# Kernel optimization log

Hardware: AMD Instinct MI355X
Metric: run time of the kernel (lower is better)

The kernel has to match this reference:

```python
import jax, jax.numpy as jnp
import numpy as np

B, S, IN = 1, 50000, 128
N = B * S
E = 800000
HID, HEADS, OUT = 64, 2, 64
NEG_SLOPE = 0.2
BN_EPS = 1e-5


def setup_inputs() -> dict:
    key = jax.random.key(0)
    ks = jax.random.split(key, 12)
    s = 0.1
    return {
        "data": jax.random.normal(ks[0], (B, S, IN), jnp.float32),
        "edge_index": jax.random.randint(ks[1], (2, E), 0, N, dtype=jnp.int64),
        "W0": jax.random.normal(ks[2], (IN, HEADS * HID), jnp.float32) * s,
        "att_src0": jax.random.normal(ks[3], (HEADS, HID), jnp.float32) * s,
        "att_dst0": jax.random.normal(ks[4], (HEADS, HID), jnp.float32) * s,
        "bias0": jnp.zeros((HEADS * HID,), jnp.float32),
        "gamma0": jnp.ones((HEADS * HID,), jnp.float32),
        "beta0": jnp.zeros((HEADS * HID,), jnp.float32),
        "W1": jax.random.normal(ks[5], (HEADS * HID, OUT), jnp.float32) * s,
        "att_src1": jax.random.normal(ks[6], (1, OUT), jnp.float32) * s,
        "att_dst1": jax.random.normal(ks[7], (1, OUT), jnp.float32) * s,
        "bias1": jnp.zeros((OUT,), jnp.float32),
    }


def gat_conv(x, edge_index, W, att_src, att_dst, bias, heads, ch, concat):
    n = x.shape[0]
    loop = jnp.arange(n, dtype=edge_index.dtype)
    src = jnp.concatenate([edge_index[0], loop])  # PyG adds self-loops by default
    dst = jnp.concatenate([edge_index[1], loop])
    h = (x @ W).reshape(n, heads, ch)  # [N,H,C]
    a_src = (h * att_src).sum(-1)  # [N,H]
    a_dst = (h * att_dst).sum(-1)  # [N,H]
    e = jax.nn.leaky_relu(a_src[src] + a_dst[dst], NEG_SLOPE)  # [Etot,H]
    m = jax.ops.segment_max(e, dst, num_segments=n)  # segment softmax over dst
    ex = jnp.exp(e - m[dst])
    denom = jax.ops.segment_sum(ex, dst, num_segments=n)
    alpha = ex / (denom[dst] + 1e-16)  # [Etot,H]
    out = jax.ops.segment_sum(h[src] * alpha[:, :, None], dst, num_segments=n)  # [N,H,C]
    out = out.reshape(n, heads * ch) if concat else out.mean(axis=1)
    return out + bias


def reference(data, edge_index, W0, att_src0, att_dst0, bias0, gamma0, beta0,
              W1, att_src1, att_dst1, bias1):
    x = data.reshape(N, IN)
    x = gat_conv(x, edge_index, W0, att_src0, att_dst0, bias0, HEADS, HID, True)
    mu = x.mean(axis=0)
    var = x.var(axis=0)
    x = (x - mu) * jax.lax.rsqrt(var + BN_EPS) * gamma0 + beta0  # BatchNorm1d (batch stats)
    x = jax.nn.elu(x)
    x = gat_conv(x, edge_index, W1, att_src1, att_dst1, bias1, 1, OUT, False)
    return x.reshape(B, S, OUT)
```

## Files before the change

kernel.cpp:

```cpp
#include <hip/hip_runtime.h>
#include <hip/hip_fp16.h>
#include <math.h>

#define N_NODES 50000
#define E_EDGES 800000
#define NEG_SLOPE 0.2f
#define BN_EPS 1e-5f

#define BK_SHIFT 9
#define NBK 98
#define L1_BLOCKS 256
#define L1_CHUNK (E_EDGES / L1_BLOCKS)
#define CNT_N (NBK * L1_BLOCKS)
#define SCG_BLOCKS ((CNT_N + 1023) / 1024)
#define STAGE_MAX 9216

typedef __attribute__((ext_vector_type(8))) _Float16 half8;
typedef __attribute__((ext_vector_type(4))) float f32x4;

__device__ __forceinline__ float lrelu(float v) { return v > 0.f ? v : NEG_SLOPE * v; }

__global__ void k_zero(float* __restrict__ bn_sum, float* __restrict__ bn_sumsq) {
  int t = threadIdx.x;
  if (t < 128) { bn_sum[t] = 0.f; bn_sumsq[t] = 0.f; }
}

__global__ void k_cvtW(const float* __restrict__ W0, const float* __restrict__ W1,
                       _Float16* __restrict__ W0t, _Float16* __restrict__ W1t) {
  int t = threadIdx.x;
  for (int idx = t; idx < 128 * 128; idx += 256) {
    int k = idx >> 7, c = idx & 127;
    W0t[c * 128 + k] = (_Float16)W0[idx];
  }
  for (int idx = t; idx < 128 * 64; idx += 256) {
    int k = idx >> 6, c = idx & 63;
    W1t[c * 128 + k] = (_Float16)W1[idx];
  }
}

__global__ __launch_bounds__(256) void k_l1hist(const int* __restrict__ dst,
                                                int* __restrict__ cnt) {
  __shared__ int lcnt[NBK];
  int t = threadIdx.x;
  if (t < NBK) lcnt[t] = 0;
  __syncthreads();
  int beg = blockIdx.x * L1_CHUNK, end = beg + L1_CHUNK;
  for (int e = beg + t; e < end; e += 256)
    atomicAdd(&lcnt[((unsigned int)dst[e]) >> BK_SHIFT], 1);
  __syncthreads();
  for (int b = t; b < NBK; b += 256) cnt[b * L1_BLOCKS + blockIdx.x] = lcnt[b];
}

__global__ __launch_bounds__(256) void k_scan1g(const int* __restrict__ cnt,
                                                int* __restrict__ tmp,
                                                int* __restrict__ bsums) {
  __shared__ int ts[256];
  int t = threadIdx.x;
  int base = blockIdx.x * 1024 + t * 4;
  int c0 = (base + 0 < CNT_N) ? cnt[base + 0] : 0;
  int c1 = (base + 1 < CNT_N) ? cnt[base + 1] : 0;
  int c2 = (base + 2 < CNT_N) ? cnt[base + 2] : 0;
  int c3 = (base + 3 < CNT_N) ? cnt[base + 3] : 0;
  int s = c0 + c1 + c2 + c3;
  ts[t] = s;
  __syncthreads();
  for (int off = 1; off < 256; off <<= 1) {
    int v = (t >= off) ? ts[t - off] : 0;
    __syncthreads();
    ts[t] += v;
    __syncthreads();
  }
  int excl = ts[t] - s;
  if (t == 255) bsums[blockIdx.x] = ts[255];
  if (base + 0 < CNT_N) tmp[base + 0] = excl;
  if (base + 1 < CNT_N) tmp[base + 1] = excl + c0;
  if (base + 2 < CNT_N) tmp[base + 2] = excl + c0 + c1;
  if (base + 3 < CNT_N) tmp[base + 3] = excl + c0 + c1 + c2;
}

__global__ void k_scan2g(int* __restrict__ bsums) {
  int t = threadIdx.x;
  int orig = (t < SCG_BLOCKS) ? bsums[t] : 0;
  int v = orig;
#pragma unroll
  for (int off = 1; off < 64; off <<= 1) {
    int u = __shfl_up(v, off);
    if (t >= off) v += u;
  }
  if (t < SCG_BLOCKS) bsums[t] = v - orig;
}

__global__ __launch_bounds__(256) void k_l1scatter(const int* __restrict__ src,
                                                   const int* __restrict__ dst,
                                                   const int* __restrict__ tmp,
                                                   const int* __restrict__ bsums,
                                                   unsigned int* __restrict__ binned) {
  __shared__ int cur[NBK];
  int t = threadIdx.x;
  for (int b = t; b < NBK; b += 256) {
    int idx = b * L1_BLOCKS + blockIdx.x;
    cur[b] = tmp[idx] + bsums[idx >> 10];
  }
  __syncthreads();
  int beg = blockIdx.x * L1_CHUNK, end = beg + L1_CHUNK;
  for (int e = beg + t; e < end; e += 256) {
    unsigned int d = (unsigned int)dst[e];
    int b = d >> BK_SHIFT;
    int p = atomicAdd(&cur[b], 1);
    binned[p] = ((unsigned int)src[e] << 16) | d;
  }
}

__global__ void k_bbase(const int* __restrict__ tmp, const int* __restrict__ bsums,
                        int* __restrict__ bucket_base) {
  int b = threadIdx.x;
  if (b < NBK) {
    int idx = b * L1_BLOCKS;
    bucket_base[b] = tmp[idx] + bsums[idx >> 10];
  }
  if (b == NBK) bucket_base[NBK] = E_EDGES;
}

__global__ __launch_bounds__(256) void k_scatter3(const int* __restrict__ bucket_base,
                                                  const unsigned int* __restrict__ binned,
                                                  int* __restrict__ row_ptr,
                                                  int* __restrict__ csr_src) {
  __shared__ int cnt[512];
  __shared__ int staging[STAGE_MAX];
  __shared__ int ts[256];
  int t = threadIdx.x;
  int b = blockIdx.x;
  int lo = b << BK_SHIFT;
  int hi = lo + 512; if (hi > N_NODES) hi = N_NODES;
  int nloc = hi - lo;
  int base = bucket_base[b];
  int end = bucket_base[b + 1];
  cnt[t] = 0; cnt[t + 256] = 0;
  __syncthreads();
  for (int i = base + t; i < end; i += 256)
    atomicAdd(&cnt[(binned[i] & 0xFFFFu) - lo], 1);
  __syncthreads();
  int c0 = cnt[2 * t], c1 = cnt[2 * t + 1];
  int pair = c0 + c1;
  ts[t] = pair;
  __syncthreads();
  for (int off = 1; off < 256; off <<= 1) {
    int v = (t >= off) ? ts[t - off] : 0;
    __syncthreads();
    ts[t] += v;
    __syncthreads();
  }
  int exclp = ts[t] - pair;
  cnt[2 * t] = exclp;
  cnt[2 * t + 1] = exclp + c0;
  if (2 * t < nloc) row_ptr[lo + 2 * t] = base + exclp;
  if (2 * t + 1 < nloc) row_ptr[lo + 2 * t + 1] = base + exclp + c0;
  if (b == NBK - 1 && t == 0) row_ptr[N_NODES] = E_EDGES;
  __syncthreads();
  for (int i = base + t; i < end; i += 256) {
    unsigned int v = binned[i];
    int d = (int)(v & 0xFFFFu) - lo;
    int p = atomicAdd(&cnt[d], 1);
    int s = (int)(v >> 16);
    if (p < STAGE_MAX) staging[p] = s;
    else csr_src[base + p] = s;
  }
  __syncthreads();
  int tot = end - base;
  int lim = tot < STAGE_MAX ? tot : STAGE_MAX;
  for (int k = t; k < lim; k += 256) csr_src[base + k] = staging[k];
}

__global__ __launch_bounds__(256) void k_gemm0m(
    const float* __restrict__ x, const _Float16* __restrict__ Wt,
    const float* __restrict__ att_s, const float* __restrict__ att_d,
    _Float16* __restrict__ h, float* __restrict__ a_src, float* __restrict__ a_dst) {
  int lane = threadIdx.x & 63;
  int wv = threadIdx.x >> 6;
  int row0 = blockIdx.x * 64 + wv * 16;
  int m = lane & 15, kg = lane >> 4;
  int arow = row0 + m;
  int arowc = arow < N_NODES ? arow : N_NODES - 1;
  f32x4 acc[8];
#pragma unroll
  for (int ct = 0; ct < 8; ct++) acc[ct] = (f32x4){0.f, 0.f, 0.f, 0.f};
#pragma unroll
  for (int kc = 0; kc < 4; kc++) {
    const float* xp = &x[(size_t)arowc * 128 + kc * 32 + kg * 8];
    float4 xa = *(const float4*)xp;
    float4 xb = *(const float4*)(xp + 4);
    half8 af = {(_Float16)xa.x, (_Float16)xa.y, (_Float16)xa.z, (_Float16)xa.w,
                (_Float16)xb.x, (_Float16)xb.y, (_Float16)xb.z, (_Float16)xb.w};
#pragma unroll
    for (int ct = 0; ct < 8; ct++) {
      half8 bf = *(const half8*)&Wt[(ct * 16 + m) * 128 + kc * 32 + kg * 8];
      acc[ct] = __builtin_amdgcn_mfma_f32_16x16x32_f16(af, bf, acc[ct], 0, 0, 0);
    }
  }
  float as[8], ad[8];
#pragma unroll
  for (int ct = 0; ct < 8; ct++) { as[ct] = att_s[ct * 16 + m]; ad[ct] = att_d[ct * 16 + m]; }
#pragma unroll
  for (int r = 0; r < 4; r++) {
    int row = row0 + kg * 4 + r;
    bool ok = row < N_NODES;
    float ps0 = 0.f, pd0 = 0.f, ps1 = 0.f, pd1 = 0.f;
#pragma unroll
    for (int ct = 0; ct < 4; ct++) { ps0 += acc[ct][r] * as[ct]; pd0 += acc[ct][r] * ad[ct]; }
#pragma unroll
    for (int ct = 4; ct < 8; ct++) { ps1 += acc[ct][r] * as[ct]; pd1 += acc[ct][r] * ad[ct]; }
#pragma unroll
    for (int msk = 1; msk <= 8; msk <<= 1) {
      ps0 += __shfl_xor(ps0, msk); pd0 += __shfl_xor(pd0, msk);
      ps1 += __shfl_xor(ps1, msk); pd1 += __shfl_xor(pd1, msk);
    }
    if (ok) {
#pragma unroll
      for (int ct = 0; ct < 8; ct++)
        h[(size_t)row * 128 + ct * 16 + m] = (_Float16)acc[ct][r];
      if (m == 0) {
        a_src[row * 2 + 0] = ps0; a_dst[row * 2 + 0] = pd0;
        a_src[row * 2 + 1] = ps1; a_dst[row * 2 + 1] = pd1;
      }
    }
  }
}

__global__ __launch_bounds__(256) void k_gemm1m(
    const float* __restrict__ y, const float* __restrict__ scale,
    const float* __restrict__ shift, const _Float16* __restrict__ Wt,
    const float* __restrict__ att_s, const float* __restrict__ att_d,
    _Float16* __restrict__ h, float* __restrict__ a_src, float* __restrict__ a_dst) {
  int lane = threadIdx.x & 63;
  int wv = threadIdx.x >> 6;
  int row0 = blockIdx.x * 64 + wv * 16;
  int m = lane & 15, kg = lane >> 4;
  int arow = row0 + m;
  int arowc = arow < N_NODES ? arow : N_NODES - 1;
  f32x4 acc[4];
#pragma unroll
  for (int ct = 0; ct < 4; ct++) acc[ct] = (f32x4){0.f, 0.f, 0.f, 0.f};
#pragma unroll
  for (int kc = 0; kc < 4; kc++) {
    int kb = kc * 32 + kg * 8;
    const float* yp = &y[(size_t)arowc * 128 + kb];
    float4 ya = *(const float4*)yp;
    float4 yb = *(const float4*)(yp + 4);
    float4 sa = *(const float4*)&scale[kb], sb = *(const float4*)&scale[kb + 4];
    float4 fa = *(const float4*)&shift[kb], fb = *(const float4*)&shift[kb + 4];
    float v[8];
    v[0] = ya.x * sa.x + fa.x; v[1] = ya.y * sa.y + fa.y;
    v[2] = ya.z * sa.z + fa.z; v[3] = ya.w * sa.w + fa.w;
    v[4] = yb.x * sb.x + fb.x; v[5] = yb.y * sb.y + fb.y;
    v[6] = yb.z * sb.z + fb.z; v[7] = yb.w * sb.w + fb.w;
    half8 af;
#pragma unroll
    for (int j = 0; j < 8; j++) {
      float e = v[j] > 0.f ? v[j] : __expf(v[j]) - 1.f;
      af[j] = (_Float16)e;
    }
#pragma unroll
    for (int ct = 0; ct < 4; ct++) {
      half8 bf = *(const half8*)&Wt[(ct * 16 + m) * 128 + kb];
      acc[ct] = __builtin_amdgcn_mfma_f32_16x16x32_f16(af, bf, acc[ct], 0, 0, 0);
    }
  }
  float as[4], ad[4];
#pragma unroll
  for (int ct = 0; ct < 4; ct++) { as[ct] = att_s[ct * 16 + m]; ad[ct] = att_d[ct * 16 + m]; }
#pragma unroll
  for (int r = 0; r < 4; r++) {
    int row = row0 + kg * 4 + r;
    bool ok = row < N_NODES;
    float ps = 0.f, pd = 0.f;
#pragma unroll
    for (int ct = 0; ct < 4; ct++) { ps += acc[ct][r] * as[ct]; pd += acc[ct][r] * ad[ct]; }
#pragma unroll
    for (int msk = 1; msk <= 8; msk <<= 1) {
      ps += __shfl_xor(ps, msk); pd += __shfl_xor(pd, msk);
    }
    if (ok) {
#pragma unroll
      for (int ct = 0; ct < 4; ct++)
        h[(size_t)row * 64 + ct * 16 + m] = (_Float16)acc[ct][r];
      if (m == 0) { a_src[row] = ps; a_dst[row] = pd; }
    }
  }
}

__global__ __launch_bounds__(256) void k_wts0(
    const int* __restrict__ row_ptr, const int* __restrict__ csr_src,
    const float* __restrict__ a_src, const float* __restrict__ a_dst,
    __half2* __restrict__ wts, float2* __restrict__ selfw) {
  int node = (blockIdx.x * blockDim.x + threadIdx.x) >> 6;
  if (node >= N_NODES) return;
  int l = threadIdx.x & 63;
  float ad0 = a_dst[node * 2], ad1 = a_dst[node * 2 + 1];
  float es0 = lrelu(a_src[node * 2] + ad0);
  float es1 = lrelu(a_src[node * 2 + 1] + ad1);
  int beg = row_ptr[node], end = row_ptr[node + 1];
  const float NEGBIG = -3.0e38f;
  float m0 = NEGBIG, s0 = 0.f, m1 = NEGBIG, s1 = 0.f;
  for (int j = beg + l; j < end; j += 64) {
    int s = csr_src[j];
    float e0 = lrelu(a_src[s * 2] + ad0);
    float e1 = lrelu(a_src[s * 2 + 1] + ad1);
    float nm0 = fmaxf(m0, e0);
    s0 = s0 * __expf(m0 - nm0) + __expf(e0 - nm0); m0 = nm0;
    float nm1 = fmaxf(m1, e1);
    s1 = s1 * __expf(m1 - nm1) + __expf(e1 - nm1); m1 = nm1;
  }
#pragma unroll
  for (int msk = 1; msk < 64; msk <<= 1) {
    float om0 = __shfl_xor(m0, msk), os0 = __shfl_xor(s0, msk);
    float nm0 = fmaxf(m0, om0);
    s0 = s0 * __expf(m0 - nm0) + os0 * __expf(om0 - nm0); m0 = nm0;
    float om1 = __shfl_xor(m1, msk), os1 = __shfl_xor(s1, msk);
    float nm1 = fmaxf(m1, om1);
    s1 = s1 * __expf(m1 - nm1) + os1 * __expf(om1 - nm1); m1 = nm1;
  }
  float fm0 = fmaxf(m0, es0);
  float d0 = s0 * __expf(m0 - fm0) + __expf(es0 - fm0);
  float fm1 = fmaxf(m1, es1);
  float d1 = s1 * __expf(m1 - fm1) + __expf(es1 - fm1);
  float inv0 = 1.f / d0, inv1 = 1.f / d1;
  for (int j = beg + l; j < end; j += 64) {
    int s = csr_src[j];
    float e0 = lrelu(a_src[s * 2] + ad0);
    float e1 = lrelu(a_src[s * 2 + 1] + ad1);
    wts[j] = __floats2half2_rn(__expf(e0 - fm0) * inv0, __expf(e1 - fm1) * inv1);
  }
  if (l == 0) selfw[node] = make_float2(__expf(es0 - fm0) * inv0, __expf(es1 - fm1) * inv1);
}

__global__ __launch_bounds__(256) void k_acc0(
    const int* __restrict__ row_ptr, const int* __restrict__ csr_src,
    const _Float16* __restrict__ h, const __half2* __restrict__ wts,
    const float2* __restrict__ selfw, const float* __restrict__ bias,
    float* __restrict__ out) {
  int node = (blockIdx.x * blockDim.x + threadIdx.x) >> 6;
  if (node >= N_NODES) return;
  int l = threadIdx.x & 63;
  int cl = l & 15, ew = l >> 4;
  int cbase = cl * 8;
  int head = cl >> 3;
  float acc[8];
#pragma unroll
  for (int k = 0; k < 8; k++) acc[k] = 0.f;
  int beg = row_ptr[node], end = row_ptr[node + 1];
  if (ew == 0) {
    float2 sw = selfw[node];
    float a = head ? sw.y : sw.x;
    half8 hv = *(const half8*)&h[(size_t)node * 128 + cbase];
#pragma unroll
    for (int k = 0; k < 8; k++) acc[k] += a * (float)hv[k];
  }
  int j = beg + ew;
  for (; j + 4 < end; j += 8) {
    int s0 = csr_src[j], s1 = csr_src[j + 4];
    __half2 w0 = wts[j], w1 = wts[j + 4];
    half8 h0v = *(const half8*)&h[(size_t)s0 * 128 + cbase];
    half8 h1v = *(const half8*)&h[(size_t)s1 * 128 + cbase];
    float a0 = head ? __high2float(w0) : __low2float(w0);
    float a1 = head ? __high2float(w1) : __low2float(w1);
#pragma unroll
    for (int k = 0; k < 8; k++) acc[k] += a0 * (float)h0v[k] + a1 * (float)h1v[k];
  }
  if (j < end) {
    int s0 = csr_src[j];
    __half2 w0 = wts[j];
    half8 h0v = *(const half8*)&h[(size_t)s0 * 128 + cbase];
    float a0 = head ? __high2float(w0) : __low2float(w0);
#pragma unroll
    for (int k = 0; k < 8; k++) acc[k] += a0 * (float)h0v[k];
  }
#pragma unroll
  for (int k = 0; k < 8; k++) {
    acc[k] += __shfl_xor(acc[k], 16);
    acc[k] += __shfl_xor(acc[k], 32);
  }
  if (ew == 0) {
    float4 b0 = *(const float4*)&bias[cbase];
    float4 b1 = *(const float4*)&bias[cbase + 4];
    float4 o0 = make_float4(acc[0] + b0.x, acc[1] + b0.y, acc[2] + b0.z, acc[3] + b0.w);
    float4 o1 = make_float4(acc[4] + b1.x, acc[5] + b1.y, acc[6] + b1.z, acc[7] + b1.w);
    *(float4*)&out[(size_t)node * 128 + cbase] = o0;
    *(float4*)&out[(size_t)node * 128 + cbase + 4] = o1;
  }
}

__global__ __launch_bounds__(256) void k_bnstats(const float* __restrict__ x,
                                                 float* __restrict__ bn_sum,
                                                 float* __restrict__ bn_sumsq) {
  int f = threadIdx.x & 127;
  int half = threadIdx.x >> 7;
  float s = 0.f, s2 = 0.f;
  for (int r = blockIdx.x * 2 + half; r < N_NODES; r += gridDim.x * 2) {
    float v = x[(size_t)r * 128 + f];
    s += v;
    s2 += v * v;
  }
  __shared__ float ls[256], ls2[256];
  ls[threadIdx.x] = s;
  ls2[threadIdx.x] = s2;
  __syncthreads();
  if (half == 0) {
    atomicAdd(&bn_sum[f], s + ls[f + 128]);
    atomicAdd(&bn_sumsq[f], s2 + ls2[f + 128]);
  }
}

__global__ void k_bnfinal(const float* __restrict__ sum, const float* __restrict__ sumsq,
                          const float* __restrict__ gamma, const float* __restrict__ beta,
                          float* __restrict__ scale, float* __restrict__ shift) {
  int f = threadIdx.x;
  float mu = sum[f] / (float)N_NODES;
  float var = sumsq[f] / (float)N_NODES - mu * mu;
  float sc = gamma[f] * rsqrtf(var + BN_EPS);
  scale[f] = sc;
  shift[f] = beta[f] - mu * sc;
}

__global__ __launch_bounds__(256) void k_wts1(
    const int* __restrict__ row_ptr, const int* __restrict__ csr_src,
    const float* __restrict__ a_src, const float* __restrict__ a_dst,
    __half* __restrict__ wts, float* __restrict__ selfw) {
  int node = (blockIdx.x * blockDim.x + threadIdx.x) >> 6;
  if (node >= N_NODES) return;
  int l = threadIdx.x & 63;
  float ad = a_dst[node];
  float es = lrelu(a_src[node] + ad);
  int beg = row_ptr[node], end = row_ptr[node + 1];
  const float NEGBIG = -3.0e38f;
  float m = NEGBIG, s = 0.f;
  for (int j = beg + l; j < end; j += 64) {
    int sn = csr_src[j];
    float e = lrelu(a_src[sn] + ad);
    float nm = fmaxf(m, e);
    s = s * __expf(m - nm) + __expf(e - nm); m = nm;
  }
#pragma unroll
  for (int msk = 1; msk < 64; msk <<= 1) {
    float om = __shfl_xor(m, msk), os = __shfl_xor(s, msk);
    float nm = fmaxf(m, om);
    s = s * __expf(m - nm) + os * __expf(om - nm); m = nm;
  }
  float fm = fmaxf(m, es);
  float d = s * __expf(m - fm) + __expf(es - fm);
  float inv = 1.f / d;
  for (int j = beg + l; j < end; j += 64) {
    int sn = csr_src[j];
    float e = lrelu(a_src[sn] + ad);
    wts[j] = __float2half_rn(__expf(e - fm) * inv);
  }
  if (l == 0) selfw[node] = __expf(es - fm) * inv;
}

__global__ __launch_bounds__(256) void k_acc1(
    const int* __restrict__ row_ptr, const int* __restrict__ csr_src,
    const _Float16* __restrict__ h, const __half* __restrict__ wts,
    const float* __restrict__ selfw, const float* __restrict__ bias,
    float* __restrict__ out) {
  int node = (blockIdx.x * blockDim.x + threadIdx.x) >> 6;
  if (node >= N_NODES) return;
  int l = threadIdx.x & 63;
  int cl = l & 7, ew = l >> 3;
  int cbase = cl * 8;
  float acc[8];
#pragma unroll
  for (int k = 0; k < 8; k++) acc[k] = 0.f;
  int beg = row_ptr[node], end = row_ptr[node + 1];
  if (ew == 0) {
    float a = selfw[node];
    half8 hv = *(const half8*)&h[(size_t)node * 64 + cbase];
#pragma unroll
    for (int k = 0; k < 8; k++) acc[k] += a * (float)hv[k];
  }
  int j = beg + ew;
  for (; j + 8 < end; j += 16) {
    int s0 = csr_src[j], s1 = csr_src[j + 8];
    float a0 = __half2float(wts[j]), a1 = __half2float(wts[j + 8]);
    half8 h0v = *(const half8*)&h[(size_t)s0 * 64 + cbase];
    half8 h1v = *(const half8*)&h[(size_t)s1 * 64 + cbase];
#pragma unroll
    for (int k = 0; k < 8; k++) acc[k] += a0 * (float)h0v[k] + a1 * (float)h1v[k];
  }
  if (j < end) {
    int s0 = csr_src[j];
    float a0 = __half2float(wts[j]);
    half8 h0v = *(const half8*)&h[(size_t)s0 * 64 + cbase];
#pragma unroll
    for (int k = 0; k < 8; k++) acc[k] += a0 * (float)h0v[k];
  }
#pragma unroll
  for (int k = 0; k < 8; k++) {
    acc[k] += __shfl_xor(acc[k], 8);
    acc[k] += __shfl_xor(acc[k], 16);
    acc[k] += __shfl_xor(acc[k], 32);
  }
  if (ew == 0) {
    float4 b0 = *(const float4*)&bias[cbase];
    float4 b1 = *(const float4*)&bias[cbase + 4];
    float4 o0 = make_float4(acc[0] + b0.x, acc[1] + b0.y, acc[2] + b0.z, acc[3] + b0.w);
    float4 o1 = make_float4(acc[4] + b1.x, acc[5] + b1.y, acc[6] + b1.z, acc[7] + b1.w);
    *(float4*)&out[(size_t)node * 64 + cbase] = o0;
    *(float4*)&out[(size_t)node * 64 + cbase + 4] = o1;
  }
}

extern "C" void kernel_launch(void* const* d_in, const int* in_sizes, int n_in,
                              void* d_out, int out_size, void* d_ws, size_t ws_size,
                              hipStream_t stream) {
  const float* data = (const float*)d_in[0];
  const int* ei = (const int*)d_in[1];
  const float* W0 = (const float*)d_in[2];
  const float* att_src0 = (const float*)d_in[3];
  const float* att_dst0 = (const float*)d_in[4];
  const float* bias0 = (const float*)d_in[5];
  const float* gamma0 = (const float*)d_in[6];
  const float* beta0 = (const float*)d_in[7];
  const float* W1 = (const float*)d_in[8];
  const float* att_src1 = (const float*)d_in[9];
  const float* att_dst1 = (const float*)d_in[10];
  const float* bias1 = (const float*)d_in[11];
  float* out = (float*)d_out;

  char* ws = (char*)d_ws;
  size_t off = 0;
  auto alloc = [&](size_t bytes) -> void* {
    void* p = ws + off;
    off = (off + bytes + 255) & ~(size_t)255;
    return p;
  };
  int* cnt = (int*)alloc((size_t)CNT_N * 4);
  int* tmp = (int*)alloc((size_t)CNT_N * 4);
  int* bsums = (int*)alloc(32 * 4);
  int* bucket_base = (int*)alloc((NBK + 1) * 4);
  int* row_ptr = (int*)alloc((N_NODES + 1) * 4);
  unsigned int* binned = (unsigned int*)alloc((size_t)E_EDGES * 4);
  int* csr_src = (int*)alloc((size_t)E_EDGES * 4);
  _Float16* W0t = (_Float16*)alloc(128 * 128 * 2);
  _Float16* W1t = (_Float16*)alloc(64 * 128 * 2);
  _Float16* h0 = (_Float16*)alloc((size_t)N_NODES * 128 * 2);
  float* a_s0 = (float*)alloc((size_t)N_NODES * 2 * 4);
  float* a_d0 = (float*)alloc((size_t)N_NODES * 2 * 4);
  __half2* wts0 = (__half2*)alloc((size_t)E_EDGES * 4);
  float2* selfw0 = (float2*)alloc((size_t)N_NODES * 8);
  float* out0 = (float*)alloc((size_t)N_NODES * 128 * 4);
  float* bn_sum = (float*)alloc(128 * 4);
  float* bn_sumsq = (float*)alloc(128 * 4);
  float* bn_scale = (float*)alloc(128 * 4);
  float* bn_shift = (float*)alloc(128 * 4);
  _Float16* h1 = h0;
  float* a_s1 = a_s0;
  float* a_d1 = a_d0;
  __half* wts1 = (__half*)wts0;
  float* selfw1 = (float*)selfw0;

  const int* srcArr = ei;
  const int* dstArr = ei + E_EDGES;

  k_zero<<<1, 128, 0, stream>>>(bn_sum, bn_sumsq);
  k_cvtW<<<1, 256, 0, stream>>>(W0, W1, W0t, W1t);
  k_l1hist<<<L1_BLOCKS, 256, 0, stream>>>(dstArr, cnt);
  k_scan1g<<<SCG_BLOCKS, 256, 0, stream>>>(cnt, tmp, bsums);
  k_scan2g<<<1, 64, 0, stream>>>(bsums);
  k_l1scatter<<<L1_BLOCKS, 256, 0, stream>>>(srcArr, dstArr, tmp, bsums, binned);
  k_bbase<<<1, 128, 0, stream>>>(tmp, bsums, bucket_base);
  k_scatter3<<<NBK, 256, 0, stream>>>(bucket_base, binned, row_ptr, csr_src);
  k_gemm0m<<<(N_NODES + 63) / 64, 256, 0, stream>>>(data, W0t, att_src0, att_dst0, h0, a_s0,
                                                    a_d0);
  k_wts0<<<(N_NODES + 3) / 4, 256, 0, stream>>>(row_ptr, csr_src, a_s0, a_d0, wts0, selfw0);
  k_acc0<<<(N_NODES + 3) / 4, 256, 0, stream>>>(row_ptr, csr_src, h0, wts0, selfw0, bias0, out0);
  k_bnstats<<<1024, 256, 0, stream>>>(out0, bn_sum, bn_sumsq);
  k_bnfinal<<<1, 128, 0, stream>>>(bn_sum, bn_sumsq, gamma0, beta0, bn_scale, bn_shift);
  k_gemm1m<<<(N_NODES + 63) / 64, 256, 0, stream>>>(out0, bn_scale, bn_shift, W1t, att_src1,
                                                    att_dst1, h1, a_s1, a_d1);
  k_wts1<<<(N_NODES + 3) / 4, 256, 0, stream>>>(row_ptr, csr_src, a_s1, a_d1, wts1, selfw1);
  k_acc1<<<(N_NODES + 3) / 4, 256, 0, stream>>>(row_ptr, csr_src, h1, wts1, selfw1, bias1, out);
}
```

Before: 330.3 us.

## Fuse softmax weight computation into aggregation kernels for both GAT layers

Merges the per-edge attention weight kernel and the aggregation kernel of each layer into one. Each wavefront computes the online softmax max and denominator, then recomputes every edge's weight inline while gathering neighbour features. This removes the fp16 weight and self-weight arrays, their global writes and reads, and two launches. The cost is recomputing exp and re-reading a_src per edge inside the aggregation loop, and the tail iterations now use predicated loads. The first pass also reads a_src as a float2.

```diff
diff --git a/kernel.cpp b/kernel.cpp
--- a/kernel.cpp
+++ b/kernel.cpp
@@ -288,10 +288,11 @@
   }
 }
 
-__global__ __launch_bounds__(256) void k_wts0(
+__global__ __launch_bounds__(256) void k_fagg0(
     const int* __restrict__ row_ptr, const int* __restrict__ csr_src,
-    const float* __restrict__ a_src, const float* __restrict__ a_dst,
-    __half2* __restrict__ wts, float2* __restrict__ selfw) {
+    const _Float16* __restrict__ h, const float* __restrict__ a_src,
+    const float* __restrict__ a_dst, const float* __restrict__ bias,
+    float* __restrict__ out) {
   int node = (blockIdx.x * blockDim.x + threadIdx.x) >> 6;
   if (node >= N_NODES) return;
   int l = threadIdx.x & 63;
@@ -303,8 +304,8 @@
   float m0 = NEGBIG, s0 = 0.f, m1 = NEGBIG, s1 = 0.f;
   for (int j = beg + l; j < end; j += 64) {
     int s = csr_src[j];
-    float e0 = lrelu(a_src[s * 2] + ad0);
-    float e1 = lrelu(a_src[s * 2 + 1] + ad1);
+    float2 asv = *(const float2*)&a_src[s * 2];
+    float e0 = lrelu(asv.x + ad0), e1 = lrelu(asv.y + ad1);
     float nm0 = fmaxf(m0, e0);
     s0 = s0 * __expf(m0 - nm0) + __expf(e0 - nm0); m0 = nm0;
     float nm1 = fmaxf(m1, e1);
@@ -319,60 +320,50 @@
     float nm1 = fmaxf(m1, om1);
     s1 = s1 * __expf(m1 - nm1) + os1 * __expf(om1 - nm1); m1 = nm1;
   }
-  float fm0 = fmaxf(m0, es0);
-  float d0 = s0 * __expf(m0 - fm0) + __expf(es0 - fm0);
-  float fm1 = fmaxf(m1, es1);
-  float d1 = s1 * __expf(m1 - fm1) + __expf(es1 - fm1);
-  float inv0 = 1.f / d0, inv1 = 1.f / d1;
-  for (int j = beg + l; j < end; j += 64) {
-    int s = csr_src[j];
-    float e0 = lrelu(a_src[s * 2] + ad0);
-    float e1 = lrelu(a_src[s * 2 + 1] + ad1);
-    wts[j] = __floats2half2_rn(__expf(e0 - fm0) * inv0, __expf(e1 - fm1) * inv1);
-  }
-  if (l == 0) selfw[node] = make_float2(__expf(es0 - fm0) * inv0, __expf(es1 - fm1) * inv1);
-}
-
-__global__ __launch_bounds__(256) void k_acc0(
-    const int* __restrict__ row_ptr, const int* __restrict__ csr_src,
-    const _Float16* __restrict__ h, const __half2* __restrict__ wts,
-    const float2* __restrict__ selfw, const float* __restrict__ bias,
-    float* __restrict__ out) {
-  int node = (blockIdx.x * blockDim.x + threadIdx.x) >> 6;
-  if (node >= N_NODES) return;
-  int l = threadIdx.x & 63;
+  float fm0 = fmaxf(m0, es0), fm1 = fmaxf(m1, es1);
+  float inv0 = 1.f / (s0 * __expf(m0 - fm0) + __expf(es0 - fm0));
+  float inv1 = 1.f / (s1 * __expf(m1 - fm1) + __expf(es1 - fm1));
   int cl = l & 15, ew = l >> 4;
   int cbase = cl * 8;
   int head = cl >> 3;
+  float adh = head ? ad1 : ad0;
+  float fmh = head ? fm1 : fm0;
+  float invh = head ? inv1 : inv0;
   float acc[8];
 #pragma unroll
   for (int k = 0; k < 8; k++) acc[k] = 0.f;
-  int beg = row_ptr[node], end = row_ptr[node + 1];
   if (ew == 0) {
-    float2 sw = selfw[node];
-    float a = head ? sw.y : sw.x;
+    float wself = head ? __expf(es1 - fm1) * inv1 : __expf(es0 - fm0) * inv0;
     half8 hv = *(const half8*)&h[(size_t)node * 128 + cbase];
 #pragma unroll
-    for (int k = 0; k < 8; k++) acc[k] += a * (float)hv[k];
-  }
-  int j = beg + ew;
-  for (; j + 4 < end; j += 8) {
-    int s0 = csr_src[j], s1 = csr_src[j + 4];
-    __half2 w0 = wts[j], w1 = wts[j + 4];
-    half8 h0v = *(const half8*)&h[(size_t)s0 * 128 + cbase];
-    half8 h1v = *(const half8*)&h[(size_t)s1 * 128 + cbase];
-    float a0 = head ? __high2float(w0) : __low2float(w0);
-    float a1 = head ? __high2float(w1) : __low2float(w1);
-#pragma unroll
-    for (int k = 0; k < 8; k++) acc[k] += a0 * (float)h0v[k] + a1 * (float)h1v[k];
-  }
-  if (j < end) {
-    int s0 = csr_src[j];
-    __half2 w0 = wts[j];
-    half8 h0v = *(const half8*)&h[(size_t)s0 * 128 + cbase];
-    float a0 = head ? __high2float(w0) : __low2float(w0);
-#pragma unroll
-    for (int k = 0; k < 8; k++) acc[k] += a0 * (float)h0v[k];
+    for (int k = 0; k < 8; k++) acc[k] += wself * (float)hv[k];
+  }
+  int deg = end - beg;
+  int nt = (deg + 3) >> 2;
+  int t = 0;
+  for (; t + 1 < nt; t += 2) {
+    int j0 = beg + t * 4 + ew, j1 = j0 + 4;
+    bool v0 = j0 < end, v1 = j1 < end;
+    int sA = v0 ? csr_src[j0] : node;
+    int sB = v1 ? csr_src[j1] : node;
+    float eA = lrelu(a_src[sA * 2 + head] + adh);
+    float eB = lrelu(a_src[sB * 2 + head] + adh);
+    float wA = v0 ? __expf(eA - fmh) * invh : 0.f;
+    float wB = v1 ? __expf(eB - fmh) * invh : 0.f;
+    half8 hA = *(const half8*)&h[(size_t)sA * 128 + cbase];
+    half8 hB = *(const half8*)&h[(size_t)sB * 128 + cbase];
+#pragma unroll
+    for (int k = 0; k < 8; k++) acc[k] += wA * (float)hA[k] + wB * (float)hB[k];
+  }
+  if (t < nt) {
+    int j0 = beg + t * 4 + ew;
+    bool v0 = j0 < end;
+    int sA = v0 ? csr_src[j0] : node;
+    float eA = lrelu(a_src[sA * 2 + head] + adh);
+    float wA = v0 ? __expf(eA - fmh) * invh : 0.f;
+    half8 hA = *(const half8*)&h[(size_t)sA * 128 + cbase];
+#pragma unroll
+    for (int k = 0; k < 8; k++) acc[k] += wA * (float)hA[k];
   }
 #pragma unroll
   for (int k = 0; k < 8; k++) {
@@ -421,10 +412,11 @@
   shift[f] = beta[f] - mu * sc;
 }
 
-__global__ __launch_bounds__(256) void k_wts1(
+__global__ __launch_bounds__(256) void k_fagg1(
     const int* __restrict__ row_ptr, const int* __restrict__ csr_src,
-    const float* __restrict__ a_src, const float* __restrict__ a_dst,
-    __half* __restrict__ wts, float* __restrict__ selfw) {
+    const _Float16* __restrict__ h, const float* __restrict__ a_src,
+    const float* __restrict__ a_dst, const float* __restrict__ bias,
+    float* __restrict__ out) {
   int node = (blockIdx.x * blockDim.x + threadIdx.x) >> 6;
   if (node >= N_NODES) return;
   int l = threadIdx.x & 63;
@@ -446,51 +438,44 @@
     s = s * __expf(m - nm) + os * __expf(om - nm); m = nm;
   }
   float fm = fmaxf(m, es);
-  float d = s * __expf(m - fm) + __expf(es - fm);
-  float inv = 1.f / d;
-  for (int j = beg + l; j < end; j += 64) {
-    int sn = csr_src[j];
-    float e = lrelu(a_src[sn] + ad);
-    wts[j] = __float2half_rn(__expf(e - fm) * inv);
-  }
-  if (l == 0) selfw[node] = __expf(es - fm) * inv;
-}
-
-__global__ __launch_bounds__(256) void k_acc1(
-    const int* __restrict__ row_ptr, const int* __restrict__ csr_src,
-    const _Float16* __restrict__ h, const __half* __restrict__ wts,
-    const float* __restrict__ selfw, const float* __restrict__ bias,
-    float* __restrict__ out) {
-  int node = (blockIdx.x * blockDim.x + threadIdx.x) >> 6;
-  if (node >= N_NODES) return;
-  int l = threadIdx.x & 63;
+  float inv = 1.f / (s * __expf(m - fm) + __expf(es - fm));
   int cl = l & 7, ew = l >> 3;
   int cbase = cl * 8;
   float acc[8];
 #pragma unroll
   for (int k = 0; k < 8; k++) acc[k] = 0.f;
-  int beg = row_ptr[node], end = row_ptr[node + 1];
   if (ew == 0) {
-    float a = selfw[node];
+    float wself = __expf(es - fm) * inv;
     half8 hv = *(const half8*)&h[(size_t)node * 64 + cbase];
 #pragma unroll
-    for (int k = 0; k < 8; k++) acc[k] += a * (float)hv[k];
-  }
-  int j = beg + ew;
-  for (; j + 8 < end; j += 16) {
-    int s0 = csr_src[j], s1 = csr_src[j + 8];
-    float a0 = __half2float(wts[j]), a1 = __half2float(wts[j + 8]);
-    half8 h0v = *(const half8*)&h[(size_t)s0 * 64 + cbase];
-    half8 h1v = *(const half8*)&h[(size_t)s1 * 64 + cbase];
-#pragma unroll
-    for (int k = 0; k < 8; k++) acc[k] += a0 * (float)h0v[k] + a1 * (float)h1v[k];
-  }
-  if (j < end) {
-    int s0 = csr_src[j];
-    float a0 = __half2float(wts[j]);
-    half8 h0v = *(const half8*)&h[(size_t)s0 * 64 + cbase];
-#pragma unroll
-    for (int k = 0; k < 8; k++) acc[k] += a0 * (float)h0v[k];
+    for (int k = 0; k < 8; k++) acc[k] += wself * (float)hv[k];
+  }
+  int deg = end - beg;
+  int nt = (deg + 7) >> 3;
+  int t = 0;
+  for (; t + 1 < nt; t += 2) {
+    int j0 = beg + t * 8 + ew, j1 = j0 + 8;
+    bool v0 = j0 < end, v1 = j1 < end;
+    int sA = v0 ? csr_src[j0] : node;
+    int sB = v1 ? csr_src[j1] : node;
+    float eA = lrelu(a_src[sA] + ad);
+    float eB = lrelu(a_src[sB] + ad);
+    float wA = v0 ? __expf(eA - fm) * inv : 0.f;
+    float wB = v1 ? __expf(eB - fm) * inv : 0.f;
+    half8 hA = *(const half8*)&h[(size_t)sA * 64 + cbase];
+    half8 hB = *(const half8*)&h[(size_t)sB * 64 + cbase];
+#pragma unroll
+    for (int k = 0; k < 8; k++) acc[k] += wA * (float)hA[k] + wB * (float)hB[k];
+  }
+  if (t < nt) {
+    int j0 = beg + t * 8 + ew;
+    bool v0 = j0 < end;
+    int sA = v0 ? csr_src[j0] : node;
+    float eA = lrelu(a_src[sA] + ad);
+    float wA = v0 ? __expf(eA - fm) * inv : 0.f;
+    half8 hA = *(const half8*)&h[(size_t)sA * 64 + cbase];
+#pragma unroll
+    for (int k = 0; k < 8; k++) acc[k] += wA * (float)hA[k];
   }
 #pragma unroll
   for (int k = 0; k < 8; k++) {
@@ -544,8 +529,6 @@
   _Float16* h0 = (_Float16*)alloc((size_t)N_NODES * 128 * 2);
   float* a_s0 = (float*)alloc((size_t)N_NODES * 2 * 4);
   float* a_d0 = (float*)alloc((size_t)N_NODES * 2 * 4);
-  __half2* wts0 = (__half2*)alloc((size_t)E_EDGES * 4);
-  float2* selfw0 = (float2*)alloc((size_t)N_NODES * 8);
   float* out0 = (float*)alloc((size_t)N_NODES * 128 * 4);
   float* bn_sum = (float*)alloc(128 * 4);
   float* bn_sumsq = (float*)alloc(128 * 4);
@@ -554,8 +537,6 @@
   _Float16* h1 = h0;
   float* a_s1 = a_s0;
   float* a_d1 = a_d0;
-  __half* wts1 = (__half*)wts0;
-  float* selfw1 = (float*)selfw0;
 
   const int* srcArr = ei;
   const int* dstArr = ei + E_EDGES;
@@ -570,12 +551,10 @@
   k_scatter3<<<NBK, 256, 0, stream>>>(bucket_base, binned, row_ptr, csr_src);
   k_gemm0m<<<(N_NODES + 63) / 64, 256, 0, stream>>>(data, W0t, att_src0, att_dst0, h0, a_s0,
                                                     a_d0);
-  k_wts0<<<(N_NODES + 3) / 4, 256, 0, stream>>>(row_ptr, csr_src, a_s0, a_d0, wts0, selfw0);
-  k_acc0<<<(N_NODES + 3) / 4, 256, 0, stream>>>(row_ptr, csr_src, h0, wts0, selfw0, bias0, out0);
+  k_fagg0<<<(N_NODES + 3) / 4, 256, 0, stream>>>(row_ptr, csr_src, h0, a_s0, a_d0, bias0, out0);
   k_bnstats<<<1024, 256, 0, stream>>>(out0, bn_sum, bn_sumsq);
   k_bnfinal<<<1, 128, 0, stream>>>(bn_sum, bn_sumsq, gamma0, beta0, bn_scale, bn_shift);
   k_gemm1m<<<(N_NODES + 63) / 64, 256, 0, stream>>>(out0, bn_scale, bn_shift, W1t, att_src1,
                                                     att_dst1, h1, a_s1, a_d1);
-  k_wts1<<<(N_NODES + 3) / 4, 256, 0, stream>>>(row_ptr, csr_src, a_s1, a_d1, wts1, selfw1);
-  k_acc1<<<(N_NODES + 3) / 4, 256, 0, stream>>>(row_ptr, csr_src, h1, wts1, selfw1, bias1, out);
-}
+  k_fagg1<<<(N_NODES + 3) / 4, 256, 0, stream>>>(row_ptr, csr_src, h1, a_s1, a_d1, bias1, out);
+}
```

Result: faster. 304.6 us (-7.8%).
